# Performance work log

Hardware: AMD Instinct MI355X
Metric: run time of the kernel (lower is better)

The kernel has to match this reference:

```python
import jax, jax.numpy as jnp
import numpy as np

B, C, N, K, O = 8, 64, 4096, 16, 64  # batch, in_channels, nodes, knn, out_channels


def setup_inputs() -> dict:
    key = jax.random.key(0)
    k1, k2, k3 = jax.random.split(key, 3)
    x = jax.random.normal(k1, (B, C, N, 1), dtype=jnp.float32)
    # edge_index[0] = source (neighbor) idx, edge_index[1] = target (center) idx
    src = jax.random.randint(k2, (B, N, K), 0, N, dtype=jnp.int32)
    dst = jnp.broadcast_to(jnp.arange(N, dtype=jnp.int32)[None, :, None], (B, N, K))
    edge_index = jnp.stack([src, dst], axis=0)  # [2, B, N, K]
    # BasicLayer([2C, O]) == Linear(2C, O, bias=True) + ReLU (norm=None)
    W = jax.random.normal(k3, (2 * C, O), dtype=jnp.float32) * (1.0 / np.sqrt(2 * C))
    b = jnp.zeros((O,), dtype=jnp.float32)
    return {"x": x, "edge_index": edge_index, "W": W, "b": b}


def reference(x, edge_index, W, b):
    Bs, Cs, Ns, _ = x.shape
    # [B, C, N, 1] -> [B*N, C] node feature matrix
    xf = x.squeeze(-1).transpose(0, 2, 1).reshape(Bs * Ns, Cs)
    # convert per-batch indices to global node ids (offset by b*N), flatten edges
    off = (jnp.arange(Bs, dtype=edge_index.dtype) * Ns)[None, :, None, None]
    ei = (edge_index + off).reshape(2, -1)  # [2, E]
    src, dst = ei[0], ei[1]
    x_i = xf[dst]          # target/center features  [E, C]
    x_j = xf[src]          # source/neighbor features [E, C]
    # EdgeConv message: MLP(concat(x_i, x_j - x_i))
    h = jax.nn.relu(jnp.concatenate([x_i, x_j - x_i], axis=-1) @ W + b)  # [E, O]
    # max-aggregate messages onto target nodes
    out = jax.ops.segment_max(h, dst, num_segments=Bs * Ns)  # [B*N, O]
    Os = out.shape[-1]
    return out.reshape(Bs, Ns, Os).transpose(0, 2, 1)[..., None]  # [B, O, N, 1]
```

## Files before the change

### kernel.cpp

```cpp
#include <hip/hip_runtime.h>
#include <hip/hip_bf16.h>


#define BB 8
#define CC 64
#define NN 4096
#define KK 16
#define OO 64

typedef __bf16 bf16x8 __attribute__((ext_vector_type(8)));
typedef float f32x4 __attribute__((ext_vector_type(4)));

union Frag { int4 i; bf16x8 v; };
union PackA { bf16x8 v; __hip_bfloat16 h[8]; };

__global__ __launch_bounds__(256, 3) void fg_gemm(
    const float* __restrict__ x, const float* __restrict__ W,
    const float* __restrict__ bias, __hip_bfloat16* __restrict__ FG) {
    __shared__ float xt[64][65];
    __shared__ int4 wfl[16][64];

    int t = threadIdx.x, w = t >> 6, l = t & 63;
    int b = blockIdx.x >> 6;
    int n0 = (blockIdx.x & 63) << 6;

    const float* xb = x + (size_t)b * CC * NN;
    #pragma unroll
    for (int it = 0; it < 4; ++it) {
        int idx = it * 256 + t;
        int c = idx >> 4, q = idx & 15;
        float4 v = *(const float4*)(xb + (size_t)c * NN + n0 + q * 4);
        xt[c][q * 4 + 0] = v.x; xt[c][q * 4 + 1] = v.y;
        xt[c][q * 4 + 2] = v.z; xt[c][q * 4 + 3] = v.w;
    }
    {
        __hip_bfloat16* wlu = (__hip_bfloat16*)wfl;
        int o = t & 63, h = t >> 6;
        #pragma unroll
        for (int kk = 0; kk < 16; ++kk) {
            int k = h * 16 + kk;
            float wa = W[k * OO + o];
            float wb = W[(64 + k) * OO + o];
            int g = (k >> 3) & 3, j = k & 7, ks = k >> 5;
            int lane = (g << 4) | (o & 15);
            int fsA = ks * 8 + (o >> 4);
            int fsB = fsA + 4;
            wlu[((fsA * 64 + lane) << 3) | j] = __float2bfloat16(wa - wb);
            wlu[((fsB * 64 + lane) << 3) | j] = __float2bfloat16(wb);
        }
    }
    __syncthreads();

    Frag wf[2][8];
    #pragma unroll
    for (int ks = 0; ks < 2; ++ks)
        #pragma unroll
        for (int ot = 0; ot < 8; ++ot)
            wf[ks][ot].i = wfl[ks * 8 + ot][l];

    f32x4 acc[8];
    #pragma unroll
    for (int ot = 0; ot < 8; ++ot) {
        float bv = (ot < 4) ? bias[ot * 16 + (l & 15)] : 0.0f;
        acc[ot] = f32x4{bv, bv, bv, bv};
    }

    int node = (w << 4) + (l & 15);
    #pragma unroll
    for (int ks = 0; ks < 2; ++ks) {
        PackA a;
        #pragma unroll
        for (int j = 0; j < 8; ++j)
            a.h[j] = __float2bfloat16(xt[ks * 32 + ((l >> 4) << 3) + j][node]);
        #pragma unroll
        for (int ot = 0; ot < 8; ++ot)
            acc[ot] = __builtin_amdgcn_mfma_f32_16x16x32_bf16(a.v, wf[ks][ot].v, acc[ot], 0, 0, 0);
    }

    size_t base = ((size_t)b * NN + n0 + (w << 4)) * 128;
    #pragma unroll
    for (int ot = 0; ot < 8; ++ot)
        #pragma unroll
        for (int r = 0; r < 4; ++r) {
            int nd = ((l >> 4) << 2) + r;
            FG[base + (size_t)nd * 128 + ot * 16 + (l & 15)] = __float2bfloat16(acc[ot][r]);
        }
}

__global__ __launch_bounds__(256, 4) void gather_max(
    const int* __restrict__ ei, const uint2* __restrict__ FGq,
    float* __restrict__ out) {
    __shared__ float otile[64][33];
    int t = threadIdx.x, w = t >> 6, l = t & 63;
    int b = blockIdx.x >> 7;
    int n0 = (blockIdx.x & 127) << 5;

    const int* srcp = ei + (size_t)b * NN * KK;
    size_t bbase = (size_t)b * NN;
    int nb = n0 + (w << 3);
    int eg = l >> 4;
    int c  = l & 15;

    int idxv[8];
    #pragma unroll
    for (int i = 0; i < 8; ++i) idxv[i] = srcp[(nb + i) * KK + c];

    uint2 fv[2];
    #pragma unroll
    for (int p = 0; p < 2; ++p) fv[p] = FGq[(bbase + nb + (p << 2) + eg) * 32 + c];

    uint2 g[8][4];
    #pragma unroll
    for (int i = 0; i < 8; ++i)
        #pragma unroll
        for (int q = 0; q < 4; ++q) {
            int vk = __shfl(idxv[i], (q << 2) | eg);
            g[i][q] = FGq[((size_t)bbase + vk) * 32 + 16 + c];
        }

    #pragma unroll
    for (int i = 0; i < 8; ++i) {
        float m0 = -3.4e38f, m1 = -3.4e38f, m2 = -3.4e38f, m3 = -3.4e38f;
        #pragma unroll
        for (int q = 0; q < 4; ++q) {
            m0 = fmaxf(m0, __uint_as_float(g[i][q].x << 16));
            m1 = fmaxf(m1, __uint_as_float(g[i][q].x & 0xffff0000u));
            m2 = fmaxf(m2, __uint_as_float(g[i][q].y << 16));
            m3 = fmaxf(m3, __uint_as_float(g[i][q].y & 0xffff0000u));
        }
        m0 = fmaxf(m0, __shfl_xor(m0, 16)); m0 = fmaxf(m0, __shfl_xor(m0, 32));
        m1 = fmaxf(m1, __shfl_xor(m1, 16)); m1 = fmaxf(m1, __shfl_xor(m1, 32));
        m2 = fmaxf(m2, __shfl_xor(m2, 16)); m2 = fmaxf(m2, __shfl_xor(m2, 32));
        m3 = fmaxf(m3, __shfl_xor(m3, 16)); m3 = fmaxf(m3, __shfl_xor(m3, 32));
        if (eg == (i & 3)) {
            uint2 f = fv[i >> 2];
            int nl = (w << 3) + i;
            otile[4 * c + 0][nl] = fmaxf(__uint_as_float(f.x << 16) + m0, 0.0f);
            otile[4 * c + 1][nl] = fmaxf(__uint_as_float(f.x & 0xffff0000u) + m1, 0.0f);
            otile[4 * c + 2][nl] = fmaxf(__uint_as_float(f.y << 16) + m2, 0.0f);
            otile[4 * c + 3][nl] = fmaxf(__uint_as_float(f.y & 0xffff0000u) + m3, 0.0f);
        }
    }
    __syncthreads();

    float* ob = out + (size_t)b * OO * NN;
    #pragma unroll
    for (int it = 0; it < 8; ++it) {
        int idx = it * 256 + t, o = idx >> 5, nn = idx & 31;
        ob[(size_t)o * NN + n0 + nn] = otile[o][nn];
    }
}

extern "C" void kernel_launch(void* const* d_in, const int* in_sizes, int n_in,
                              void* d_out, int out_size, void* d_ws, size_t ws_size,
                              hipStream_t stream) {
    const float* x    = (const float*)d_in[0];
    const int*   ei   = (const int*)d_in[1];
    const float* W    = (const float*)d_in[2];
    const float* bias = (const float*)d_in[3];
    float* out = (float*)d_out;

    __hip_bfloat16* FG = (__hip_bfloat16*)d_ws;

    hipLaunchKernelGGL(fg_gemm, dim3(BB * (NN / 64)), dim3(256), 0, stream,
                       x, W, bias, FG);
    hipLaunchKernelGGL(gather_max, dim3(BB * (NN / 32)), dim3(256), 0, stream,
                       ei, (const uint2*)FG, out);
}
```

Baseline: 24.58 us.

## Fuse GEMM and gather-max into persistent XCD-affine kernel with atomic work queues

Merges the two kernels into one persistent kernel of 512 blocks. Each block reads its XCC_ID hardware register and uses it to pick a batch, so all of a batch's FG table is produced and consumed on one XCD and its L2. Work tiles come from per-batch atomic counters, and a per-batch done counter serves as a spin barrier between the producer and consumer phases. This removes a kernel launch boundary and aims to keep gathers L2-local, at the cost of an extra memset, atomics, spin-waiting, and reliance on how blocks are spread across XCDs.

Measured after the change: 77.31 us. 215% more time.

```diff
diff --git a/kernel.cpp b/kernel.cpp
--- a/kernel.cpp
+++ b/kernel.cpp
@@ -14,27 +14,31 @@
 union Frag { int4 i; bf16x8 v; };
 union PackA { bf16x8 v; __hip_bfloat16 h[8]; };
 
-__global__ __launch_bounds__(256, 3) void fg_gemm(
-    const float* __restrict__ x, const float* __restrict__ W,
-    const float* __restrict__ bias, __hip_bfloat16* __restrict__ FG) {
-    __shared__ float xt[64][65];
-    __shared__ int4 wfl[16][64];
+static constexpr size_t FG_BYTES = (size_t)BB * NN * 128 * 2;
+static constexpr int GRID = 512;
+
+__global__ __launch_bounds__(256, 2) void edgeconv_xcd(
+    const float* __restrict__ x, const int* __restrict__ ei,
+    const float* __restrict__ W, const float* __restrict__ bias,
+    float* __restrict__ out, __hip_bfloat16* __restrict__ FG,
+    unsigned* __restrict__ ctr) {
+    __shared__ union {
+        struct { float xt[64][65]; int4 wfl[16][64]; } p;
+        float ot[64][33];
+    } sm;
+    __shared__ unsigned s_t;
 
     int t = threadIdx.x, w = t >> 6, l = t & 63;
-    int b = blockIdx.x >> 6;
-    int n0 = (blockIdx.x & 63) << 6;
+    unsigned xreg;
+    asm volatile("s_getreg_b32 %0, hwreg(HW_REG_XCC_ID)" : "=s"(xreg));
+    int b = (int)(xreg & 7);
 
-    const float* xb = x + (size_t)b * CC * NN;
-    #pragma unroll
-    for (int it = 0; it < 4; ++it) {
-        int idx = it * 256 + t;
-        int c = idx >> 4, q = idx & 15;
-        float4 v = *(const float4*)(xb + (size_t)c * NN + n0 + q * 4);
-        xt[c][q * 4 + 0] = v.x; xt[c][q * 4 + 1] = v.y;
-        xt[c][q * 4 + 2] = v.z; xt[c][q * 4 + 3] = v.w;
-    }
+    unsigned* prod_ctr  = ctr;
+    unsigned* prod_done = ctr + 8;
+    unsigned* cons_ctr  = ctr + 16;
+
     {
-        __hip_bfloat16* wlu = (__hip_bfloat16*)wfl;
+        __hip_bfloat16* wlu = (__hip_bfloat16*)sm.p.wfl;
         int o = t & 63, h = t >> 6;
         #pragma unroll
         for (int kk = 0; kk < 16; ++kk) {
@@ -50,104 +54,128 @@
         }
     }
     __syncthreads();
-
     Frag wf[2][8];
     #pragma unroll
     for (int ks = 0; ks < 2; ++ks)
         #pragma unroll
         for (int ot = 0; ot < 8; ++ot)
-            wf[ks][ot].i = wfl[ks * 8 + ot][l];
+            wf[ks][ot].i = sm.p.wfl[ks * 8 + ot][l];
+    float bvv[8];
+    #pragma unroll
+    for (int ot = 0; ot < 8; ++ot) bvv[ot] = (ot < 4) ? bias[ot * 16 + (l & 15)] : 0.0f;
 
-    f32x4 acc[8];
-    #pragma unroll
-    for (int ot = 0; ot < 8; ++ot) {
-        float bv = (ot < 4) ? bias[ot * 16 + (l & 15)] : 0.0f;
-        acc[ot] = f32x4{bv, bv, bv, bv};
+    const float* xb = x + (size_t)b * CC * NN;
+    __hip_bfloat16* FGb = FG + (size_t)b * NN * 128;
+
+    for (;;) {
+        __syncthreads();
+        if (t == 0) s_t = atomicAdd(&prod_ctr[b], 1u);
+        __syncthreads();
+        unsigned tt = s_t;
+        if (tt >= 64u) break;
+        int n0 = (int)tt << 6;
+
+        #pragma unroll
+        for (int it = 0; it < 4; ++it) {
+            int idx = it * 256 + t, c = idx >> 4, q = idx & 15;
+            float4 v = *(const float4*)(xb + (size_t)c * NN + n0 + q * 4);
+            sm.p.xt[c][q * 4 + 0] = v.x; sm.p.xt[c][q * 4 + 1] = v.y;
+            sm.p.xt[c][q * 4 + 2] = v.z; sm.p.xt[c][q * 4 + 3] = v.w;
+        }
+        __syncthreads();
+
+        f32x4 acc[8];
+        #pragma unroll
+        for (int ot = 0; ot < 8; ++ot) acc[ot] = f32x4{bvv[ot], bvv[ot], bvv[ot], bvv[ot]};
+        int node = (w << 4) + (l & 15);
+        #pragma unroll
+        for (int ks = 0; ks < 2; ++ks) {
+            PackA a;
+            #pragma unroll
+            for (int j = 0; j < 8; ++j)
+                a.h[j] = __float2bfloat16(sm.p.xt[ks * 32 + ((l >> 4) << 3) + j][node]);
+            #pragma unroll
+            for (int ot = 0; ot < 8; ++ot)
+                acc[ot] = __builtin_amdgcn_mfma_f32_16x16x32_bf16(a.v, wf[ks][ot].v, acc[ot], 0, 0, 0);
+        }
+        size_t base = ((size_t)n0 + (w << 4)) * 128;
+        #pragma unroll
+        for (int ot = 0; ot < 8; ++ot)
+            #pragma unroll
+            for (int r = 0; r < 4; ++r) {
+                int nd = ((l >> 4) << 2) + r;
+                FGb[base + (size_t)nd * 128 + ot * 16 + (l & 15)] = __float2bfloat16(acc[ot][r]);
+            }
+        asm volatile("s_waitcnt vmcnt(0)");
+        __syncthreads();
+        if (t == 0) atomicAdd(&prod_done[b], 1u);
     }
 
-    int node = (w << 4) + (l & 15);
-    #pragma unroll
-    for (int ks = 0; ks < 2; ++ks) {
-        PackA a;
-        #pragma unroll
-        for (int j = 0; j < 8; ++j)
-            a.h[j] = __float2bfloat16(xt[ks * 32 + ((l >> 4) << 3) + j][node]);
-        #pragma unroll
-        for (int ot = 0; ot < 8; ++ot)
-            acc[ot] = __builtin_amdgcn_mfma_f32_16x16x32_bf16(a.v, wf[ks][ot].v, acc[ot], 0, 0, 0);
-    }
-
-    size_t base = ((size_t)b * NN + n0 + (w << 4)) * 128;
-    #pragma unroll
-    for (int ot = 0; ot < 8; ++ot)
-        #pragma unroll
-        for (int r = 0; r < 4; ++r) {
-            int nd = ((l >> 4) << 2) + r;
-            FG[base + (size_t)nd * 128 + ot * 16 + (l & 15)] = __float2bfloat16(acc[ot][r]);
-        }
-}
-
-__global__ __launch_bounds__(256, 4) void gather_max(
-    const int* __restrict__ ei, const uint2* __restrict__ FGq,
-    float* __restrict__ out) {
-    __shared__ float otile[64][33];
-    int t = threadIdx.x, w = t >> 6, l = t & 63;
-    int b = blockIdx.x >> 7;
-    int n0 = (blockIdx.x & 127) << 5;
-
-    const int* srcp = ei + (size_t)b * NN * KK;
-    size_t bbase = (size_t)b * NN;
-    int nb = n0 + (w << 3);
-    int eg = l >> 4;
-    int c  = l & 15;
-
-    int idxv[8];
-    #pragma unroll
-    for (int i = 0; i < 8; ++i) idxv[i] = srcp[(nb + i) * KK + c];
-
-    uint2 fv[2];
-    #pragma unroll
-    for (int p = 0; p < 2; ++p) fv[p] = FGq[(bbase + nb + (p << 2) + eg) * 32 + c];
-
-    uint2 g[8][4];
-    #pragma unroll
-    for (int i = 0; i < 8; ++i)
-        #pragma unroll
-        for (int q = 0; q < 4; ++q) {
-            int vk = __shfl(idxv[i], (q << 2) | eg);
-            g[i][q] = FGq[((size_t)bbase + vk) * 32 + 16 + c];
-        }
-
-    #pragma unroll
-    for (int i = 0; i < 8; ++i) {
-        float m0 = -3.4e38f, m1 = -3.4e38f, m2 = -3.4e38f, m3 = -3.4e38f;
-        #pragma unroll
-        for (int q = 0; q < 4; ++q) {
-            m0 = fmaxf(m0, __uint_as_float(g[i][q].x << 16));
-            m1 = fmaxf(m1, __uint_as_float(g[i][q].x & 0xffff0000u));
-            m2 = fmaxf(m2, __uint_as_float(g[i][q].y << 16));
-            m3 = fmaxf(m3, __uint_as_float(g[i][q].y & 0xffff0000u));
-        }
-        m0 = fmaxf(m0, __shfl_xor(m0, 16)); m0 = fmaxf(m0, __shfl_xor(m0, 32));
-        m1 = fmaxf(m1, __shfl_xor(m1, 16)); m1 = fmaxf(m1, __shfl_xor(m1, 32));
-        m2 = fmaxf(m2, __shfl_xor(m2, 16)); m2 = fmaxf(m2, __shfl_xor(m2, 32));
-        m3 = fmaxf(m3, __shfl_xor(m3, 16)); m3 = fmaxf(m3, __shfl_xor(m3, 32));
-        if (eg == (i & 3)) {
-            uint2 f = fv[i >> 2];
-            int nl = (w << 3) + i;
-            otile[4 * c + 0][nl] = fmaxf(__uint_as_float(f.x << 16) + m0, 0.0f);
-            otile[4 * c + 1][nl] = fmaxf(__uint_as_float(f.x & 0xffff0000u) + m1, 0.0f);
-            otile[4 * c + 2][nl] = fmaxf(__uint_as_float(f.y << 16) + m2, 0.0f);
-            otile[4 * c + 3][nl] = fmaxf(__uint_as_float(f.y & 0xffff0000u) + m3, 0.0f);
-        }
+    if (t == 0) {
+        while (atomicAdd(&prod_done[b], 0u) < 64u) __builtin_amdgcn_s_sleep(32);
     }
     __syncthreads();
 
+    const int* srcp = ei + (size_t)b * NN * KK;
+    const uint2* FGq = (const uint2*)FGb;
     float* ob = out + (size_t)b * OO * NN;
-    #pragma unroll
-    for (int it = 0; it < 8; ++it) {
-        int idx = it * 256 + t, o = idx >> 5, nn = idx & 31;
-        ob[(size_t)o * NN + n0 + nn] = otile[o][nn];
+
+    for (;;) {
+        __syncthreads();
+        if (t == 0) s_t = atomicAdd(&cons_ctr[b], 1u);
+        __syncthreads();
+        unsigned tt = s_t;
+        if (tt >= 128u) break;
+        int n0 = (int)tt << 5;
+        int nb = n0 + (w << 3);
+        int eg = l >> 4, c = l & 15;
+
+        int idxv[8];
+        #pragma unroll
+        for (int i = 0; i < 8; ++i) idxv[i] = srcp[(nb + i) * KK + c];
+
+        uint2 fv[2];
+        #pragma unroll
+        for (int p = 0; p < 2; ++p) fv[p] = FGq[(size_t)(nb + (p << 2) + eg) * 32 + c];
+
+        uint2 g[8][4];
+        #pragma unroll
+        for (int i = 0; i < 8; ++i)
+            #pragma unroll
+            for (int q = 0; q < 4; ++q) {
+                int vk = __shfl(idxv[i], (q << 2) | eg);
+                g[i][q] = FGq[(size_t)vk * 32 + 16 + c];
+            }
+
+        #pragma unroll
+        for (int i = 0; i < 8; ++i) {
+            float m0 = -3.4e38f, m1 = -3.4e38f, m2 = -3.4e38f, m3 = -3.4e38f;
+            #pragma unroll
+            for (int q = 0; q < 4; ++q) {
+                m0 = fmaxf(m0, __uint_as_float(g[i][q].x << 16));
+                m1 = fmaxf(m1, __uint_as_float(g[i][q].x & 0xffff0000u));
+                m2 = fmaxf(m2, __uint_as_float(g[i][q].y << 16));
+                m3 = fmaxf(m3, __uint_as_float(g[i][q].y & 0xffff0000u));
+            }
+            m0 = fmaxf(m0, __shfl_xor(m0, 16)); m0 = fmaxf(m0, __shfl_xor(m0, 32));
+            m1 = fmaxf(m1, __shfl_xor(m1, 16)); m1 = fmaxf(m1, __shfl_xor(m1, 32));
+            m2 = fmaxf(m2, __shfl_xor(m2, 16)); m2 = fmaxf(m2, __shfl_xor(m2, 32));
+            m3 = fmaxf(m3, __shfl_xor(m3, 16)); m3 = fmaxf(m3, __shfl_xor(m3, 32));
+            if (eg == (i & 3)) {
+                uint2 f = fv[i >> 2];
+                int nl = (w << 3) + i;
+                sm.ot[4 * c + 0][nl] = fmaxf(__uint_as_float(f.x << 16) + m0, 0.0f);
+                sm.ot[4 * c + 1][nl] = fmaxf(__uint_as_float(f.x & 0xffff0000u) + m1, 0.0f);
+                sm.ot[4 * c + 2][nl] = fmaxf(__uint_as_float(f.y << 16) + m2, 0.0f);
+                sm.ot[4 * c + 3][nl] = fmaxf(__uint_as_float(f.y & 0xffff0000u) + m3, 0.0f);
+            }
+        }
+        __syncthreads();
+        #pragma unroll
+        for (int it = 0; it < 8; ++it) {
+            int idx = it * 256 + t, o = idx >> 5, nn = idx & 31;
+            ob[(size_t)o * NN + n0 + nn] = sm.ot[o][nn];
+        }
     }
 }
 
@@ -161,9 +189,9 @@
     float* out = (float*)d_out;
 
     __hip_bfloat16* FG = (__hip_bfloat16*)d_ws;
+    unsigned* ctr = (unsigned*)((char*)d_ws + FG_BYTES);
 
-    hipLaunchKernelGGL(fg_gemm, dim3(BB * (NN / 64)), dim3(256), 0, stream,
-                       x, W, bias, FG);
-    hipLaunchKernelGGL(gather_max, dim3(BB * (NN / 32)), dim3(256), 0, stream,
-                       ei, (const uint2*)FG, out);
+    hipMemsetAsync(ctr, 0, 128, stream);
+    hipLaunchKernelGGL(edgeconv_xcd, dim3(GRID), dim3(256), 0, stream,
+                       x, ei, W, bias, out, FG, ctr);
 }
```

## Move center-node F GEMM into gather kernel, halve intermediate workspace

Applied to the files above, without the earlier changes.

The first kernel now computes only the neighbor projection G = x·W_b and writes a 64-wide bf16 buffer instead of a 128-wide one. The center term F = x·(W_a−W_b)+bias is recomputed inside the gather kernel with MFMA from an x tile in shared memory and kept in fp32 in LDS. This halves the intermediate write and avoids re-reading F from global memory. In exchange the gather kernel carries extra shared memory, a weight repack, an extra barrier and a small GEMM per block, which may reduce occupancy.

Result: no change. 24.41 us (-0.7%).

```diff
diff --git a/kernel.cpp b/kernel.cpp
--- a/kernel.cpp
+++ b/kernel.cpp
@@ -14,11 +14,11 @@
 union Frag { int4 i; bf16x8 v; };
 union PackA { bf16x8 v; __hip_bfloat16 h[8]; };
 
-__global__ __launch_bounds__(256, 3) void fg_gemm(
+__global__ __launch_bounds__(256, 3) void g_gemm(
     const float* __restrict__ x, const float* __restrict__ W,
-    const float* __restrict__ bias, __hip_bfloat16* __restrict__ FG) {
+    __hip_bfloat16* __restrict__ G) {
     __shared__ float xt[64][65];
-    __shared__ int4 wfl[16][64];
+    __shared__ int4 wfl[8][64];
 
     int t = threadIdx.x, w = t >> 6, l = t & 63;
     int b = blockIdx.x >> 6;
@@ -27,8 +27,7 @@
     const float* xb = x + (size_t)b * CC * NN;
     #pragma unroll
     for (int it = 0; it < 4; ++it) {
-        int idx = it * 256 + t;
-        int c = idx >> 4, q = idx & 15;
+        int idx = it * 256 + t, c = idx >> 4, q = idx & 15;
         float4 v = *(const float4*)(xb + (size_t)c * NN + n0 + q * 4);
         xt[c][q * 4 + 0] = v.x; xt[c][q * 4 + 1] = v.y;
         xt[c][q * 4 + 2] = v.z; xt[c][q * 4 + 3] = v.w;
@@ -39,31 +38,25 @@
         #pragma unroll
         for (int kk = 0; kk < 16; ++kk) {
             int k = h * 16 + kk;
-            float wa = W[k * OO + o];
             float wb = W[(64 + k) * OO + o];
-            int g = (k >> 3) & 3, j = k & 7, ks = k >> 5;
-            int lane = (g << 4) | (o & 15);
-            int fsA = ks * 8 + (o >> 4);
-            int fsB = fsA + 4;
-            wlu[((fsA * 64 + lane) << 3) | j] = __float2bfloat16(wa - wb);
-            wlu[((fsB * 64 + lane) << 3) | j] = __float2bfloat16(wb);
-        }
-    }
-    __syncthreads();
-
-    Frag wf[2][8];
+            int gq = (k >> 3) & 3, j = k & 7, ks = k >> 5;
+            int lane = (gq << 4) | (o & 15);
+            int fs = ks * 4 + (o >> 4);
+            wlu[((fs * 64 + lane) << 3) | j] = __float2bfloat16(wb);
+        }
+    }
+    __syncthreads();
+
+    Frag wf[2][4];
     #pragma unroll
     for (int ks = 0; ks < 2; ++ks)
         #pragma unroll
-        for (int ot = 0; ot < 8; ++ot)
-            wf[ks][ot].i = wfl[ks * 8 + ot][l];
-
-    f32x4 acc[8];
-    #pragma unroll
-    for (int ot = 0; ot < 8; ++ot) {
-        float bv = (ot < 4) ? bias[ot * 16 + (l & 15)] : 0.0f;
-        acc[ot] = f32x4{bv, bv, bv, bv};
-    }
+        for (int ot = 0; ot < 4; ++ot)
+            wf[ks][ot].i = wfl[ks * 4 + ot][l];
+
+    f32x4 acc[4];
+    #pragma unroll
+    for (int ot = 0; ot < 4; ++ot) acc[ot] = f32x4{0.f, 0.f, 0.f, 0.f};
 
     int node = (w << 4) + (l & 15);
     #pragma unroll
@@ -73,49 +66,100 @@
         for (int j = 0; j < 8; ++j)
             a.h[j] = __float2bfloat16(xt[ks * 32 + ((l >> 4) << 3) + j][node]);
         #pragma unroll
-        for (int ot = 0; ot < 8; ++ot)
+        for (int ot = 0; ot < 4; ++ot)
             acc[ot] = __builtin_amdgcn_mfma_f32_16x16x32_bf16(a.v, wf[ks][ot].v, acc[ot], 0, 0, 0);
     }
 
-    size_t base = ((size_t)b * NN + n0 + (w << 4)) * 128;
-    #pragma unroll
-    for (int ot = 0; ot < 8; ++ot)
+    size_t base = ((size_t)b * NN + n0 + (w << 4)) * 64;
+    #pragma unroll
+    for (int ot = 0; ot < 4; ++ot)
         #pragma unroll
         for (int r = 0; r < 4; ++r) {
             int nd = ((l >> 4) << 2) + r;
-            FG[base + (size_t)nd * 128 + ot * 16 + (l & 15)] = __float2bfloat16(acc[ot][r]);
+            G[base + (size_t)nd * 64 + ot * 16 + (l & 15)] = __float2bfloat16(acc[ot][r]);
         }
 }
 
 __global__ __launch_bounds__(256, 4) void gather_max(
-    const int* __restrict__ ei, const uint2* __restrict__ FGq,
-    float* __restrict__ out) {
-    __shared__ float otile[64][33];
+    const float* __restrict__ x, const int* __restrict__ ei,
+    const float* __restrict__ W, const float* __restrict__ bias,
+    const uint2* __restrict__ Gq, float* __restrict__ out) {
+    __shared__ union { float xt[64][33]; float ot_[64][33]; } sm;
+    __shared__ int4 wfl[8][64];
+    __shared__ float Fl[32][65];
+
     int t = threadIdx.x, w = t >> 6, l = t & 63;
     int b = blockIdx.x >> 7;
     int n0 = (blockIdx.x & 127) << 5;
 
+    const float* xb = x + (size_t)b * CC * NN;
+    #pragma unroll
+    for (int it = 0; it < 8; ++it) {
+        int idx = it * 256 + t, c = idx >> 5, nn = idx & 31;
+        sm.xt[c][nn] = xb[(size_t)c * NN + n0 + nn];
+    }
+    {
+        __hip_bfloat16* wlu = (__hip_bfloat16*)wfl;
+        int o = t & 63, h = t >> 6;
+        #pragma unroll
+        for (int kk = 0; kk < 16; ++kk) {
+            int k = h * 16 + kk;
+            float v = W[k * OO + o] - W[(64 + k) * OO + o];
+            int gq = (k >> 3) & 3, j = k & 7, ks = k >> 5;
+            int lane = (gq << 4) | (o & 15);
+            int fs = ks * 4 + (o >> 4);
+            wlu[((fs * 64 + lane) << 3) | j] = __float2bfloat16(v);
+        }
+    }
     const int* srcp = ei + (size_t)b * NN * KK;
+    int nb = n0 + (w << 3);
+    int eg = l >> 4, c = l & 15;
+    int idxv[8];
+    #pragma unroll
+    for (int i = 0; i < 8; ++i) idxv[i] = srcp[(nb + i) * KK + c];
+    __syncthreads();
+
+    {
+        int ng = (w & 1) << 4;
+        int ob = (w >> 1) << 1;
+        Frag wfA[2][2];
+        #pragma unroll
+        for (int ks = 0; ks < 2; ++ks)
+            #pragma unroll
+            for (int oo = 0; oo < 2; ++oo)
+                wfA[ks][oo].i = wfl[ks * 4 + ob + oo][l];
+        f32x4 acc[2];
+        #pragma unroll
+        for (int oo = 0; oo < 2; ++oo) {
+            float bv = bias[(ob + oo) * 16 + (l & 15)];
+            acc[oo] = f32x4{bv, bv, bv, bv};
+        }
+        #pragma unroll
+        for (int ks = 0; ks < 2; ++ks) {
+            PackA a;
+            #pragma unroll
+            for (int j = 0; j < 8; ++j)
+                a.h[j] = __float2bfloat16(sm.xt[ks * 32 + ((l >> 4) << 3) + j][ng + (l & 15)]);
+            #pragma unroll
+            for (int oo = 0; oo < 2; ++oo)
+                acc[oo] = __builtin_amdgcn_mfma_f32_16x16x32_bf16(a.v, wfA[ks][oo].v, acc[oo], 0, 0, 0);
+        }
+        #pragma unroll
+        for (int oo = 0; oo < 2; ++oo)
+            #pragma unroll
+            for (int r = 0; r < 4; ++r)
+                Fl[ng + ((l >> 4) << 2) + r][(ob + oo) * 16 + (l & 15)] = acc[oo][r];
+    }
+    __syncthreads();
+
     size_t bbase = (size_t)b * NN;
-    int nb = n0 + (w << 3);
-    int eg = l >> 4;
-    int c  = l & 15;
-
-    int idxv[8];
-    #pragma unroll
-    for (int i = 0; i < 8; ++i) idxv[i] = srcp[(nb + i) * KK + c];
-
-    uint2 fv[2];
-    #pragma unroll
-    for (int p = 0; p < 2; ++p) fv[p] = FGq[(bbase + nb + (p << 2) + eg) * 32 + c];
-
     uint2 g[8][4];
     #pragma unroll
     for (int i = 0; i < 8; ++i)
         #pragma unroll
         for (int q = 0; q < 4; ++q) {
             int vk = __shfl(idxv[i], (q << 2) | eg);
-            g[i][q] = FGq[((size_t)bbase + vk) * 32 + 16 + c];
+            g[i][q] = Gq[((size_t)bbase + vk) * 16 + c];
         }
 
     #pragma unroll
@@ -133,21 +177,20 @@
         m2 = fmaxf(m2, __shfl_xor(m2, 16)); m2 = fmaxf(m2, __shfl_xor(m2, 32));
         m3 = fmaxf(m3, __shfl_xor(m3, 16)); m3 = fmaxf(m3, __shfl_xor(m3, 32));
         if (eg == (i & 3)) {
-            uint2 f = fv[i >> 2];
             int nl = (w << 3) + i;
-            otile[4 * c + 0][nl] = fmaxf(__uint_as_float(f.x << 16) + m0, 0.0f);
-            otile[4 * c + 1][nl] = fmaxf(__uint_as_float(f.x & 0xffff0000u) + m1, 0.0f);
-            otile[4 * c + 2][nl] = fmaxf(__uint_as_float(f.y << 16) + m2, 0.0f);
-            otile[4 * c + 3][nl] = fmaxf(__uint_as_float(f.y & 0xffff0000u) + m3, 0.0f);
-        }
-    }
-    __syncthreads();
-
-    float* ob = out + (size_t)b * OO * NN;
+            sm.ot_[4 * c + 0][nl] = fmaxf(Fl[nl][4 * c + 0] + m0, 0.0f);
+            sm.ot_[4 * c + 1][nl] = fmaxf(Fl[nl][4 * c + 1] + m1, 0.0f);
+            sm.ot_[4 * c + 2][nl] = fmaxf(Fl[nl][4 * c + 2] + m2, 0.0f);
+            sm.ot_[4 * c + 3][nl] = fmaxf(Fl[nl][4 * c + 3] + m3, 0.0f);
+        }
+    }
+    __syncthreads();
+
+    float* ob2 = out + (size_t)b * OO * NN;
     #pragma unroll
     for (int it = 0; it < 8; ++it) {
         int idx = it * 256 + t, o = idx >> 5, nn = idx & 31;
-        ob[(size_t)o * NN + n0 + nn] = otile[o][nn];
+        ob2[(size_t)o * NN + n0 + nn] = sm.ot_[o][nn];
     }
 }
 
@@ -160,10 +203,9 @@
     const float* bias = (const float*)d_in[3];
     float* out = (float*)d_out;
 
-    __hip_bfloat16* FG = (__hip_bfloat16*)d_ws;
-
-    hipLaunchKernelGGL(fg_gemm, dim3(BB * (NN / 64)), dim3(256), 0, stream,
-                       x, W, bias, FG);
+    __hip_bfloat16* G = (__hip_bfloat16*)d_ws;
+
+    hipLaunchKernelGGL(g_gemm, dim3(BB * (NN / 64)), dim3(256), 0, stream, x, W, G);
     hipLaunchKernelGGL(gather_max, dim3(BB * (NN / 32)), dim3(256), 0, stream,
-                       ei, (const uint2*)FG, out);
+                       x, ei, W, bias, (const uint2*)G, out);
 }
```
